# Kernel tuning notes

Measured on AMD Instinct MI355X. Metric: run time of the kernel, lower is better.

## Reference

```python
import jax, jax.numpy as jnp
import numpy as np

EMBED_DIM = 1024
NUM_HEADS = 16
HEAD_DIM = EMBED_DIM // NUM_HEADS


def setup_inputs() -> dict:
    key = jax.random.key(0)
    k1, k2, k3, k4 = jax.random.split(key, 4)
    S, B = 2048, 2
    x = jax.random.normal(k1, (S, B, EMBED_DIM), dtype=jnp.float32)
    # xavier_uniform for in_proj_weight [3E, E]
    limit_in = float(np.sqrt(6.0 / (3 * EMBED_DIM + EMBED_DIM)))
    in_proj_weight = jax.random.uniform(k2, (3 * EMBED_DIM, EMBED_DIM), minval=-limit_in, maxval=limit_in, dtype=jnp.float32)
    in_proj_bias = jnp.zeros((3 * EMBED_DIM,), dtype=jnp.float32)
    # out_proj: nn.Linear default init (kaiming-uniform-ish); use uniform of similar scale
    limit_out = float(np.sqrt(1.0 / EMBED_DIM))
    out_proj_weight = jax.random.uniform(k3, (EMBED_DIM, EMBED_DIM), minval=-limit_out, maxval=limit_out, dtype=jnp.float32)
    out_proj_bias = jnp.zeros((EMBED_DIM,), dtype=jnp.float32)
    return {
        "x": x,
        "in_proj_weight": in_proj_weight,
        "in_proj_bias": in_proj_bias,
        "out_proj_weight": out_proj_weight,
        "out_proj_bias": out_proj_bias,
    }


def reference(x, in_proj_weight, in_proj_bias, out_proj_weight, out_proj_bias):
    S, B, E = x.shape
    H, D = NUM_HEADS, HEAD_DIM
    scaling = float(D) ** -0.5
    # fused QKV projection: [S, B, 3E]
    qkv = jnp.einsum("sbe,fe->sbf", x, in_proj_weight) + in_proj_bias
    q, k, v = jnp.split(qkv, 3, axis=-1)
    q = q * scaling
    # [S, B, E] -> [B*H, S, D]
    def to_heads(t):
        return t.reshape(S, B * H, D).transpose(1, 0, 2)
    q, k, v = to_heads(q), to_heads(k), to_heads(v)
    # attention scores [B*H, S, S]
    scores = jnp.einsum("btd,bsd->bts", q, k)
    weights = jax.nn.softmax(scores, axis=-1)
    # dropout p=0.0 -> identity
    attn = jnp.einsum("bts,bsd->btd", weights, v)  # [B*H, S, D]
    attn = attn.transpose(1, 0, 2).reshape(S, B, E)
    out = jnp.einsum("sbe,fe->sbf", attn, out_proj_weight) + out_proj_bias
    return out
```

## Files before the change

kernel.cpp:

```cpp
#include <hip/hip_runtime.h>

typedef __bf16 bf16_t;
typedef __attribute__((ext_vector_type(8))) __bf16 bf16x8;
typedef __attribute__((ext_vector_type(4))) __bf16 bf16x4;
typedef __attribute__((ext_vector_type(4))) float f32x4;
typedef __attribute__((ext_vector_type(16))) float f32x16;

#define MFMA16(a, b, c) __builtin_amdgcn_mfma_f32_16x16x32_bf16((a), (b), (c), 0, 0, 0)
#define MFMA32(a, b, c) __builtin_amdgcn_mfma_f32_32x32x16_bf16((a), (b), (c), 0, 0, 0)
#define LOG2E 1.44269504088896f

__device__ __forceinline__ void async16(const bf16_t* g, bf16_t* l) {
    __builtin_amdgcn_global_load_lds(
        (const __attribute__((address_space(1))) unsigned int*)g,
        (__attribute__((address_space(3))) unsigned int*)l, 16, 0, 0);
}

__device__ __forceinline__ unsigned pack2(float a, float b) {
    union { bf16_t e[2]; unsigned u; } x;
    x.e[0] = (bf16_t)a; x.e[1] = (bf16_t)b;
    return x.u;
}

__global__ __launch_bounds__(256) void conv3(
    const float* __restrict__ s0, const float* __restrict__ s1,
    const float* __restrict__ s2, bf16_t* __restrict__ dst,
    int n0, int n1)
{
    const int i = (blockIdx.x * 256 + threadIdx.x) * 8;
    const float* src;
    int off;
    if (i < n0)           { src = s0; off = 0; }
    else if (i < n0 + n1) { src = s1; off = n0; }
    else                  { src = s2; off = n0 + n1; }
    const float4 a = *reinterpret_cast<const float4*>(src + i - off);
    const float4 b = *reinterpret_cast<const float4*>(src + i - off + 4);
    bf16x8 o;
    o[0] = (bf16_t)a.x; o[1] = (bf16_t)a.y; o[2] = (bf16_t)a.z; o[3] = (bf16_t)a.w;
    o[4] = (bf16_t)b.x; o[5] = (bf16_t)b.y; o[6] = (bf16_t)b.z; o[7] = (bf16_t)b.w;
    *reinterpret_cast<bf16x8*>(dst + i) = o;
}

__global__ __launch_bounds__(256) void vtrans(
    const bf16_t* __restrict__ qkv, bf16_t* __restrict__ vT, int B)
{
    const int bh = blockIdx.x, b = bh >> 4, h = bh & 15;
    const int s0 = blockIdx.y * 64;
    __shared__ bf16_t Ls[64][65];
    const int t = threadIdx.x;
    const int sl = t & 63, dc = t >> 6;
#pragma unroll
    for (int pass = 0; pass < 2; pass++) {
        const int d8 = dc + pass * 4;
        bf16x8 v = *reinterpret_cast<const bf16x8*>(
            qkv + (size_t)((s0 + sl) * B + b) * 3072 + 2048 + h * 64 + d8 * 8);
#pragma unroll
        for (int j = 0; j < 8; j++) Ls[sl][d8 * 8 + j] = v[j];
    }
    __syncthreads();
#pragma unroll
    for (int pass = 0; pass < 2; pass++) {
        const int cid = t + pass * 256;
        const int d = cid >> 3, cs = cid & 7;
        bf16x8 o;
#pragma unroll
        for (int j = 0; j < 8; j++) o[j] = Ls[cs * 8 + j][d];
        *reinterpret_cast<bf16x8*>(
            vT + (size_t)(bh * 64 + d) * 2048 + s0 + cs * 8) = o;
    }
}

template <int MT, bool F32OUT>
__global__ __launch_bounds__(256, 3) void gemm_nt_lds(
    const bf16_t* __restrict__ W, const bf16_t* __restrict__ X,
    const float* __restrict__ bias, void* __restrict__ Cv,
    int N, int K, int scale_lim, float qscale, int fpx)
{
    constexpr int NJ = MT / 32;
    __shared__ bf16_t As[2][128 * 32];
    __shared__ bf16_t Bs[2][MT * 32];

    const int lane = threadIdx.x & 63;
    const int wv   = threadIdx.x >> 6;
    const int l15  = lane & 15;
    const int qd   = lane >> 4;

    const int id = blockIdx.x;
    const int x8 = id & 7, k = id >> 3;
    const int fb = ((k % fpx) * 8 + x8) * 128;
    const int mb = (k / fpx) * MT;
    const int fw = (wv & 1) * 64;
    const int mw = (wv >> 1) * (MT / 2);

    f32x4 acc[4][NJ] = {};

    auto stage = [&](int set, int k0) {
#pragma unroll
        for (int t = 0; t < 2; t++) {
            const int p = (wv * 2 + t) * 64 + lane;
            const int r = p >> 2, cl = (p & 3) ^ (r & 3);
            async16(W + (size_t)(fb + r) * K + k0 + cl * 8,
                    &As[set][(wv * 2 + t) * 512]);
        }
#pragma unroll
        for (int t = 0; t < MT / 64; t++) {
            const int p = (wv * (MT / 64) + t) * 64 + lane;
            const int r = p >> 2, cl = (p & 3) ^ (r & 3);
            async16(X + (size_t)(mb + r) * K + k0 + cl * 8,
                    &Bs[set][(wv * (MT / 64) + t) * 512]);
        }
    };

    stage(0, 0);
    int set = 0;
    for (int k0 = 0; k0 < K; k0 += 32) {
        __syncthreads();
        if (k0 + 32 < K) stage(set ^ 1, k0 + 32);

        const int s3 = l15 & 3;
        bf16x8 a[4], bb[NJ];
#pragma unroll
        for (int i = 0; i < 4; i++)
            a[i] = *reinterpret_cast<const bf16x8*>(
                &As[set][(fw + i * 16 + l15) * 32 + ((qd ^ s3) * 8)]);
#pragma unroll
        for (int j = 0; j < NJ; j++)
            bb[j] = *reinterpret_cast<const bf16x8*>(
                &Bs[set][(mw + j * 16 + l15) * 32 + ((qd ^ s3) * 8)]);
#pragma unroll
        for (int i = 0; i < 4; i++)
#pragma unroll
            for (int j = 0; j < NJ; j++)
                acc[i][j] = MFMA16(a[i], bb[j], acc[i][j]);
        set ^= 1;
    }

    const float scale = (fb < scale_lim) ? qscale : 1.0f;
#pragma unroll
    for (int i = 0; i < 4; i++) {
        const int f0 = fb + fw + i * 16 + qd * 4;
        float bs[4];
#pragma unroll
        for (int r = 0; r < 4; r++) bs[r] = bias[f0 + r];
#pragma unroll
        for (int j = 0; j < NJ; j++) {
            const int m = mb + mw + j * 16 + l15;
            if (F32OUT) {
                float4 o;
                o.x = (acc[i][j][0] + bs[0]) * scale;
                o.y = (acc[i][j][1] + bs[1]) * scale;
                o.z = (acc[i][j][2] + bs[2]) * scale;
                o.w = (acc[i][j][3] + bs[3]) * scale;
                *reinterpret_cast<float4*>((float*)Cv + (size_t)m * N + f0) = o;
            } else {
                bf16x4 o;
#pragma unroll
                for (int r = 0; r < 4; r++)
                    o[r] = (bf16_t)((acc[i][j][r] + bs[r]) * scale);
                *reinterpret_cast<bf16x4*>((bf16_t*)Cv + (size_t)m * N + f0) = o;
            }
        }
    }
}

__global__ __launch_bounds__(256, 2) void flash_attn(
    const bf16_t* __restrict__ qkv, const bf16_t* __restrict__ vT,
    bf16_t* __restrict__ attn, int S, int B)
{
    const int E3 = 3072, E = 1024;
    const int bh = blockIdx.x, b = bh >> 4, h = bh & 15;
    const int tid = threadIdx.x, lane = tid & 63, wv = tid >> 6;
    const int qw = wv & 1;
    const int pr = wv >> 1;
    const int l31 = lane & 31, half = lane >> 5;

    __shared__ bf16_t Kt[2][2][64 * 64];
    __shared__ bf16_t Vt[2][2][64 * 64];
    __shared__ float  lsh[2][64];

    const int q0 = blockIdx.y * 128 + qw * 64;

    bf16x8 qf[2][4];
#pragma unroll
    for (int qt = 0; qt < 2; qt++) {
        const bf16_t* qp = qkv + (size_t)((q0 + qt * 32 + l31) * B + b) * E3 + h * 64;
#pragma unroll
        for (int ks = 0; ks < 4; ks++)
            qf[qt][ks] = *reinterpret_cast<const bf16x8*>(qp + ks * 16 + half * 8);
    }

    f32x16 oacc[2][2] = {};
    float lrun[2] = {0.0f, 0.0f};

    auto stage = [&](int set, int kv) {
#pragma unroll
        for (int t = 0; t < 4; t++) {
            const int p = (qw * 4 + t) * 64 + lane;
            const int r = p >> 3, cl = (p & 7) ^ (r & 7);
            async16(qkv + (size_t)((kv + r) * B + b) * E3 + E + h * 64 + cl * 8,
                    &Kt[pr][set][(qw * 4 + t) * 512]);
            async16(vT + (size_t)(bh * 64 + r) * 2048 + kv + cl * 8,
                    &Vt[pr][set][(qw * 4 + t) * 512]);
        }
    };

    const int kvbase = pr * (S / 2);
    const int NIT = S / 128;

    stage(0, kvbase);
    int set = 0;
    for (int it = 0; it < NIT; it++) {
        __syncthreads();
        if (it + 1 < NIT) stage(set ^ 1, kvbase + (it + 1) * 64);

        const bf16_t* K_ = Kt[pr][set];
        const bf16_t* V_ = Vt[pr][set];

        union PF { unsigned u[4]; bf16x8 v; };
        PF pf[2][4];
#pragma unroll
        for (int nt = 0; nt < 2; nt++) {
            const int r = nt * 32 + l31;
            const int r7 = r & 7;
            bf16x8 kf[4];
#pragma unroll
            for (int ks = 0; ks < 4; ks++)
                kf[ks] = *reinterpret_cast<const bf16x8*>(
                    K_ + r * 64 + (((ks * 2 + half) ^ r7) * 8));
#pragma unroll
            for (int qt = 0; qt < 2; qt++) {
                f32x16 st = {};
#pragma unroll
                for (int ks = 0; ks < 4; ks++)
                    st = MFMA32(kf[ks], qf[qt][ks], st);
                float ls = 0.0f;
                unsigned q8[8];
#pragma unroll
                for (int g = 0; g < 4; g++) {
                    const float p0 = __builtin_amdgcn_exp2f(st[4 * g]);
                    const float p1 = __builtin_amdgcn_exp2f(st[4 * g + 1]);
                    const float p2 = __builtin_amdgcn_exp2f(st[4 * g + 2]);
                    const float p3 = __builtin_amdgcn_exp2f(st[4 * g + 3]);
                    ls += (p0 + p1) + (p2 + p3);
                    q8[2 * g]     = pack2(p0, p1);
                    q8[2 * g + 1] = pack2(p2, p3);
                }
                lrun[qt] += ls;
                unsigned x8[8];
#pragma unroll
                for (int k = 0; k < 8; k++) x8[k] = __shfl_xor((int)q8[k], 32);
                pf[qt][nt * 2 + 0].u[0] = half ? x8[2] : q8[0];
                pf[qt][nt * 2 + 0].u[1] = half ? x8[3] : q8[1];
                pf[qt][nt * 2 + 0].u[2] = half ? q8[2] : x8[0];
                pf[qt][nt * 2 + 0].u[3] = half ? q8[3] : x8[1];
                pf[qt][nt * 2 + 1].u[0] = half ? x8[6] : q8[4];
                pf[qt][nt * 2 + 1].u[1] = half ? x8[7] : q8[5];
                pf[qt][nt * 2 + 1].u[2] = half ? q8[6] : x8[4];
                pf[qt][nt * 2 + 1].u[3] = half ? q8[7] : x8[5];
            }
        }
#pragma unroll
        for (int kn = 0; kn < 4; kn++)
#pragma unroll
            for (int dt = 0; dt < 2; dt++) {
                const int d = dt * 32 + l31;
                bf16x8 vf = *reinterpret_cast<const bf16x8*>(
                    V_ + d * 64 + (((kn * 2 + half) ^ (d & 7)) * 8));
                oacc[0][dt] = MFMA32(vf, pf[0][kn].v, oacc[0][dt]);
                oacc[1][dt] = MFMA32(vf, pf[1][kn].v, oacc[1][dt]);
            }
        set ^= 1;
    }

    __syncthreads();
    float lr[2];
#pragma unroll
    for (int qt = 0; qt < 2; qt++) lr[qt] = lrun[qt] + __shfl_xor(lrun[qt], 32);

    float* fo = reinterpret_cast<float*>(&Kt[0][0][0]) + qw * 4096;

    if (pr == 1) {
#pragma unroll
        for (int qt = 0; qt < 2; qt++) {
            const int ql = qt * 32 + l31;
            lsh[qw][ql] = lr[qt];
#pragma unroll
            for (int dt = 0; dt < 2; dt++)
#pragma unroll
                for (int g = 0; g < 4; g++)
#pragma unroll
                    for (int r = 0; r < 4; r++) {
                        const int d = dt * 32 + g * 8 + half * 4 + r;
                        fo[d * 64 + ql] = oacc[qt][dt][4 * g + r];
                    }
        }
    }
    __syncthreads();
    if (pr == 0) {
#pragma unroll
        for (int qt = 0; qt < 2; qt++) {
            const int ql = qt * 32 + l31;
            const float inv = 1.0f / (lr[qt] + lsh[qw][ql]);
            const int qrow = q0 + qt * 32 + l31;
#pragma unroll
            for (int dt = 0; dt < 2; dt++)
#pragma unroll
                for (int g = 0; g < 4; g++) {
                    bf16x4 o;
#pragma unroll
                    for (int r = 0; r < 4; r++) {
                        const int d = dt * 32 + g * 8 + half * 4 + r;
                        o[r] = (bf16_t)((oacc[qt][dt][4 * g + r] + fo[d * 64 + ql]) * inv);
                    }
                    *reinterpret_cast<bf16x4*>(attn + (size_t)(qrow * B + b) * E +
                                               h * 64 + dt * 32 + g * 8 + half * 4) = o;
                }
        }
    }
}

extern "C" void kernel_launch(void* const* d_in, const int* in_sizes, int n_in,
                              void* d_out, int out_size, void* d_ws, size_t ws_size,
                              hipStream_t stream) {
    const float* x  = (const float*)d_in[0];
    const float* wi = (const float*)d_in[1];
    const float* bi = (const float*)d_in[2];
    const float* wo = (const float*)d_in[3];
    const float* bo = (const float*)d_in[4];
    float* out = (float*)d_out;

    const int S = 2048, B = 2, E = 1024;
    const int M = S * B;

    bf16_t* xb   = (bf16_t*)d_ws;
    bf16_t* wib  = xb  + (size_t)M * E;
    bf16_t* wob  = wib + (size_t)3 * E * E;
    bf16_t* qkv  = wob + (size_t)E * E;
    bf16_t* attn = qkv + (size_t)M * 3 * E;
    bf16_t* vT   = xb;

    const int n0 = M * E, n1 = 3 * E * E, n2 = E * E;
    conv3<<<(n0 + n1 + n2) / 8 / 256, 256, 0, stream>>>(x, wi, wo, xb, n0, n1);

    gemm_nt_lds<128, false><<<(3 * E / 128) * (M / 128), 256, 0, stream>>>(
        wib, xb, bi, qkv, 3 * E, E, E, 0.125f * LOG2E, (3 * E / 128) / 8);

    vtrans<<<dim3(B * 16, S / 64), 256, 0, stream>>>(qkv, vT, B);

    flash_attn<<<dim3(B * 16, S / 128), 256, 0, stream>>>(qkv, vT, attn, S, B);

    gemm_nt_lds<64, true><<<(E / 128) * (M / 64), 256, 0, stream>>>(
        wob, attn, bo, out, E, E, 0, 1.0f, (E / 128) / 8);
}
```

Before: 199.1 us.

## Split flash attention query rows across 8 waves and use permlane32 swap

Measured after the change: 235.3 us. 1.18x slower.

```diff
diff --git a/kernel.cpp b/kernel.cpp
--- a/kernel.cpp
+++ b/kernel.cpp
@@ -5,6 +5,7 @@
 typedef __attribute__((ext_vector_type(4))) __bf16 bf16x4;
 typedef __attribute__((ext_vector_type(4))) float f32x4;
 typedef __attribute__((ext_vector_type(16))) float f32x16;
+typedef __attribute__((ext_vector_type(2))) unsigned uint2v;
 
 #define MFMA16(a, b, c) __builtin_amdgcn_mfma_f32_16x16x32_bf16((a), (b), (c), 0, 0, 0)
 #define MFMA32(a, b, c) __builtin_amdgcn_mfma_f32_32x32x16_bf16((a), (b), (c), 0, 0, 0)
@@ -20,6 +21,11 @@
     union { bf16_t e[2]; unsigned u; } x;
     x.e[0] = (bf16_t)a; x.e[1] = (bf16_t)b;
     return x.u;
+}
+
+__device__ __forceinline__ void pl32swap(unsigned& a, unsigned& b) {
+    uint2v r = __builtin_amdgcn_permlane32_swap(a, b, false, false);
+    a = r[0]; b = r[1];
 }
 
 __global__ __launch_bounds__(256) void conv3(
@@ -163,44 +169,43 @@
     }
 }
 
-__global__ __launch_bounds__(256, 2) void flash_attn(
+__global__ __launch_bounds__(512, 4) void flash_attn(
     const bf16_t* __restrict__ qkv, const bf16_t* __restrict__ vT,
     bf16_t* __restrict__ attn, int S, int B)
 {
     const int E3 = 3072, E = 1024;
     const int bh = blockIdx.x, b = bh >> 4, h = bh & 15;
     const int tid = threadIdx.x, lane = tid & 63, wv = tid >> 6;
-    const int qw = wv & 1;
-    const int pr = wv >> 1;
+    const int qs = wv & 3;
+    const int pr = wv >> 2;
     const int l31 = lane & 31, half = lane >> 5;
 
     __shared__ bf16_t Kt[2][2][64 * 64];
     __shared__ bf16_t Vt[2][2][64 * 64];
-    __shared__ float  lsh[2][64];
-
-    const int q0 = blockIdx.y * 128 + qw * 64;
-
-    bf16x8 qf[2][4];
-#pragma unroll
-    for (int qt = 0; qt < 2; qt++) {
-        const bf16_t* qp = qkv + (size_t)((q0 + qt * 32 + l31) * B + b) * E3 + h * 64;
+    __shared__ float  lsh[128];
+
+    const int q0 = blockIdx.y * 128 + qs * 32;
+
+    bf16x8 qf[4];
+    {
+        const bf16_t* qp = qkv + (size_t)((q0 + l31) * B + b) * E3 + h * 64;
 #pragma unroll
         for (int ks = 0; ks < 4; ks++)
-            qf[qt][ks] = *reinterpret_cast<const bf16x8*>(qp + ks * 16 + half * 8);
-    }
-
-    f32x16 oacc[2][2] = {};
-    float lrun[2] = {0.0f, 0.0f};
+            qf[ks] = *reinterpret_cast<const bf16x8*>(qp + ks * 16 + half * 8);
+    }
+
+    f32x16 oacc[2] = {};
+    float lrun = 0.0f;
 
     auto stage = [&](int set, int kv) {
 #pragma unroll
-        for (int t = 0; t < 4; t++) {
-            const int p = (qw * 4 + t) * 64 + lane;
+        for (int t = 0; t < 2; t++) {
+            const int p = (qs * 2 + t) * 64 + lane;
             const int r = p >> 3, cl = (p & 7) ^ (r & 7);
             async16(qkv + (size_t)((kv + r) * B + b) * E3 + E + h * 64 + cl * 8,
-                    &Kt[pr][set][(qw * 4 + t) * 512]);
+                    &Kt[pr][set][(qs * 2 + t) * 512]);
             async16(vT + (size_t)(bh * 64 + r) * 2048 + kv + cl * 8,
-                    &Vt[pr][set][(qw * 4 + t) * 512]);
+                    &Vt[pr][set][(qs * 2 + t) * 512]);
         }
     };
 
@@ -217,7 +222,7 @@
         const bf16_t* V_ = Vt[pr][set];
 
         union PF { unsigned u[4]; bf16x8 v; };
-        PF pf[2][4];
+        PF pf[4];
 #pragma unroll
         for (int nt = 0; nt < 2; nt++) {
             const int r = nt * 32 + l31;
@@ -227,38 +232,33 @@
             for (int ks = 0; ks < 4; ks++)
                 kf[ks] = *reinterpret_cast<const bf16x8*>(
                     K_ + r * 64 + (((ks * 2 + half) ^ r7) * 8));
-#pragma unroll
-            for (int qt = 0; qt < 2; qt++) {
-                f32x16 st = {};
-#pragma unroll
-                for (int ks = 0; ks < 4; ks++)
-                    st = MFMA32(kf[ks], qf[qt][ks], st);
-                float ls = 0.0f;
-                unsigned q8[8];
-#pragma unroll
-                for (int g = 0; g < 4; g++) {
-                    const float p0 = __builtin_amdgcn_exp2f(st[4 * g]);
-                    const float p1 = __builtin_amdgcn_exp2f(st[4 * g + 1]);
-                    const float p2 = __builtin_amdgcn_exp2f(st[4 * g + 2]);
-                    const float p3 = __builtin_amdgcn_exp2f(st[4 * g + 3]);
-                    ls += (p0 + p1) + (p2 + p3);
-                    q8[2 * g]     = pack2(p0, p1);
-                    q8[2 * g + 1] = pack2(p2, p3);
-                }
-                lrun[qt] += ls;
-                unsigned x8[8];
-#pragma unroll
-                for (int k = 0; k < 8; k++) x8[k] = __shfl_xor((int)q8[k], 32);
-                pf[qt][nt * 2 + 0].u[0] = half ? x8[2] : q8[0];
-                pf[qt][nt * 2 + 0].u[1] = half ? x8[3] : q8[1];
-                pf[qt][nt * 2 + 0].u[2] = half ? q8[2] : x8[0];
-                pf[qt][nt * 2 + 0].u[3] = half ? q8[3] : x8[1];
-                pf[qt][nt * 2 + 1].u[0] = half ? x8[6] : q8[4];
-                pf[qt][nt * 2 + 1].u[1] = half ? x8[7] : q8[5];
-                pf[qt][nt * 2 + 1].u[2] = half ? q8[6] : x8[4];
-                pf[qt][nt * 2 + 1].u[3] = half ? q8[7] : x8[5];
+            f32x16 st = {};
+            __builtin_amdgcn_s_setprio(1);
+#pragma unroll
+            for (int ks = 0; ks < 4; ks++)
+                st = MFMA32(kf[ks], qf[ks], st);
+            __builtin_amdgcn_s_setprio(0);
+            float ls = 0.0f;
+            unsigned q8[8];
+#pragma unroll
+            for (int g = 0; g < 4; g++) {
+                const float p0 = __builtin_amdgcn_exp2f(st[4 * g]);
+                const float p1 = __builtin_amdgcn_exp2f(st[4 * g + 1]);
+                const float p2 = __builtin_amdgcn_exp2f(st[4 * g + 2]);
+                const float p3 = __builtin_amdgcn_exp2f(st[4 * g + 3]);
+                ls += (p0 + p1) + (p2 + p3);
+                q8[2 * g]     = pack2(p0, p1);
+                q8[2 * g + 1] = pack2(p2, p3);
             }
-        }
+            lrun += ls;
+            pl32swap(q8[0], q8[2]); pl32swap(q8[1], q8[3]);
+            pl32swap(q8[4], q8[6]); pl32swap(q8[5], q8[7]);
+            pf[nt * 2 + 0].u[0] = q8[0]; pf[nt * 2 + 0].u[1] = q8[1];
+            pf[nt * 2 + 0].u[2] = q8[2]; pf[nt * 2 + 0].u[3] = q8[3];
+            pf[nt * 2 + 1].u[0] = q8[4]; pf[nt * 2 + 1].u[1] = q8[5];
+            pf[nt * 2 + 1].u[2] = q8[6]; pf[nt * 2 + 1].u[3] = q8[7];
+        }
+        __builtin_amdgcn_s_setprio(1);
 #pragma unroll
         for (int kn = 0; kn < 4; kn++)
 #pragma unroll
@@ -266,56 +266,46 @@
                 const int d = dt * 32 + l31;
                 bf16x8 vf = *reinterpret_cast<const bf16x8*>(
                     V_ + d * 64 + (((kn * 2 + half) ^ (d & 7)) * 8));
-                oacc[0][dt] = MFMA32(vf, pf[0][kn].v, oacc[0][dt]);
-                oacc[1][dt] = MFMA32(vf, pf[1][kn].v, oacc[1][dt]);
+                oacc[dt] = MFMA32(vf, pf[kn].v, oacc[dt]);
             }
+        __builtin_amdgcn_s_setprio(0);
         set ^= 1;
     }
 
     __syncthreads();
-    float lr[2];
-#pragma unroll
-    for (int qt = 0; qt < 2; qt++) lr[qt] = lrun[qt] + __shfl_xor(lrun[qt], 32);
-
-    float* fo = reinterpret_cast<float*>(&Kt[0][0][0]) + qw * 4096;
+    const float lr = lrun + __shfl_xor(lrun, 32);
+
+    float* fo = reinterpret_cast<float*>(&Kt[0][0][0]) + qs * 2048;
 
     if (pr == 1) {
-#pragma unroll
-        for (int qt = 0; qt < 2; qt++) {
-            const int ql = qt * 32 + l31;
-            lsh[qw][ql] = lr[qt];
-#pragma unroll
-            for (int dt = 0; dt < 2; dt++)
-#pragma unroll
-                for (int g = 0; g < 4; g++)
-#pragma unroll
-                    for (int r = 0; r < 4; r++) {
-                        const int d = dt * 32 + g * 8 + half * 4 + r;
-                        fo[d * 64 + ql] = oacc[qt][dt][4 * g + r];
-                    }
-        }
+        lsh[qs * 32 + l31] = lr;
+#pragma unroll
+        for (int dt = 0; dt < 2; dt++)
+#pragma unroll
+            for (int g = 0; g < 4; g++)
+#pragma unroll
+                for (int r = 0; r < 4; r++) {
+                    const int d = dt * 32 + g * 8 + half * 4 + r;
+                    fo[d * 32 + l31] = oacc[dt][4 * g + r];
+                }
     }
     __syncthreads();
     if (pr == 0) {
-#pragma unroll
-        for (int qt = 0; qt < 2; qt++) {
-            const int ql = qt * 32 + l31;
-            const float inv = 1.0f / (lr[qt] + lsh[qw][ql]);
-            const int qrow = q0 + qt * 32 + l31;
-#pragma unroll
-            for (int dt = 0; dt < 2; dt++)
-#pragma unroll
-                for (int g = 0; g < 4; g++) {
-                    bf16x4 o;
-#pragma unroll
-                    for (int r = 0; r < 4; r++) {
-                        const int d = dt * 32 + g * 8 + half * 4 + r;
-                        o[r] = (bf16_t)((oacc[qt][dt][4 * g + r] + fo[d * 64 + ql]) * inv);
-                    }
-                    *reinterpret_cast<bf16x4*>(attn + (size_t)(qrow * B + b) * E +
-                                               h * 64 + dt * 32 + g * 8 + half * 4) = o;
+        const float inv = 1.0f / (lr + lsh[qs * 32 + l31]);
+        const int qrow = q0 + l31;
+#pragma unroll
+        for (int dt = 0; dt < 2; dt++)
+#pragma unroll
+            for (int g = 0; g < 4; g++) {
+                bf16x4 o;
+#pragma unroll
+                for (int r = 0; r < 4; r++) {
+                    const int d = dt * 32 + g * 8 + half * 4 + r;
+                    o[r] = (bf16_t)((oacc[dt][4 * g + r] + fo[d * 32 + l31]) * inv);
                 }
-        }
+                *reinterpret_cast<bf16x4*>(attn + (size_t)(qrow * B + b) * E +
+                                           h * 64 + dt * 32 + g * 8 + half * 4) = o;
+            }
     }
 }
 
@@ -347,7 +337,7 @@
 
     vtrans<<<dim3(B * 16, S / 64), 256, 0, stream>>>(qkv, vT, B);
 
-    flash_attn<<<dim3(B * 16, S / 128), 256, 0, stream>>>(qkv, vT, attn, S, B);
+    flash_attn<<<dim3(B * 16, S / 128), 512, 0, stream>>>(qkv, vT, attn, S, B);
 
     gemm_nt_lds<64, true><<<(E / 128) * (M / 64), 256, 0, stream>>>(
         wob, attn, bo, out, E, E, 0, 1.0f, (E / 128) / 8);
```
